# Optimization experiments

Hardware: AMD Instinct MI355X
Metric: run time of the kernel (lower is better)

The kernel has to match this reference:

```python
import jax, jax.numpy as jnp
import numpy as np

N = 50000      # nodes
E = 800000     # edges
R = 8          # relations
DIN, DH, DOUT = 128, 128, 64
EPS = 1e-5     # BatchNorm eps


def setup_inputs() -> dict:
    key = jax.random.key(0)
    ks = jax.random.split(key, 24)
    w = lambda k, shape, fan_in: jax.random.normal(k, shape, jnp.float32) / np.sqrt(fan_in)
    x = jax.random.normal(ks[0], (N, DIN), jnp.float32)
    edge_index = jax.random.randint(ks[1], (2, E), 0, N, dtype=jnp.int64)
    edge_type = jax.random.randint(ks[2], (E,), 0, R, dtype=jnp.int64)
    return {
        "x": x, "edge_index": edge_index, "edge_type": edge_type,
        # layer 1: RGCN(DIN->DH) + BN
        "W1": w(ks[3], (R, DIN, DH), DIN), "Wr1": w(ks[4], (DIN, DH), DIN), "b1": jnp.zeros((DH,), jnp.float32),
        "g1": jnp.ones((DH,), jnp.float32), "be1": jnp.zeros((DH,), jnp.float32),
        "rm1": 0.1 * jax.random.normal(ks[5], (DH,), jnp.float32),
        "rv1": jax.random.uniform(ks[6], (DH,), jnp.float32, 0.5, 1.5),
        # layer 2: RGCN(DH->DH) + BN
        "W2": w(ks[7], (R, DH, DH), DH), "Wr2": w(ks[8], (DH, DH), DH), "b2": jnp.zeros((DH,), jnp.float32),
        "g2": jnp.ones((DH,), jnp.float32), "be2": jnp.zeros((DH,), jnp.float32),
        "rm2": 0.1 * jax.random.normal(ks[9], (DH,), jnp.float32),
        "rv2": jax.random.uniform(ks[10], (DH,), jnp.float32, 0.5, 1.5),
        # layer 3: RGCN(DH->DOUT)
        "W3": w(ks[11], (R, DH, DOUT), DH), "Wr3": w(ks[12], (DH, DOUT), DH), "b3": jnp.zeros((DOUT,), jnp.float32),
    }


def rgcn_layer(x, W, Wroot, b, src, dst, et):
    # PyG RGCNConv: per-relation linear transform, per-relation MEAN aggregation
    # over incoming edges, plus root transform and bias.
    nR, nN, H = W.shape[0], x.shape[0], W.shape[2]
    h = jnp.einsum('nd,rdh->rnh', x, W)          # [R,N,H] per-relation transform
    msg = h[et, src]                             # [E,H] gather per edge
    seg = dst * nR + et                          # segment key = (node, relation)
    sums = jax.ops.segment_sum(msg, seg, num_segments=nN * nR)
    cnt = jax.ops.segment_sum(jnp.ones((seg.shape[0],), x.dtype), seg, num_segments=nN * nR)
    mean = sums / jnp.maximum(cnt, 1.0)[:, None]
    agg = mean.reshape(nN, nR, H).sum(axis=1)    # sum over relations
    return agg + x @ Wroot + b


def batchnorm(x, g, b, rm, rv):
    # eval-mode BatchNorm1d with running stats
    return (x - rm) * jax.lax.rsqrt(rv + EPS) * g + b


def reference(x, edge_index, edge_type,
              W1, Wr1, b1, g1, be1, rm1, rv1,
              W2, Wr2, b2, g2, be2, rm2, rv2,
              W3, Wr3, b3):
    src, dst = edge_index[0], edge_index[1]
    h = rgcn_layer(x, W1, Wr1, b1, src, dst, edge_type)
    h = jax.nn.relu(batchnorm(h, g1, be1, rm1, rv1))  # dropout: eval mode = identity
    h = rgcn_layer(h, W2, Wr2, b2, src, dst, edge_type)
    h = jax.nn.relu(batchnorm(h, g2, be2, rm2, rv2))
    h = rgcn_layer(h, W3, Wr3, b3, src, dst, edge_type)
    return jax.nn.sigmoid(h)
```

## Files before the change

### kernel.cpp

```cpp
#include <hip/hip_runtime.h>

typedef _Float16 f16;
typedef __attribute__((ext_vector_type(8))) _Float16 half8;
typedef __attribute__((ext_vector_type(2))) _Float16 half2v;
typedef __attribute__((ext_vector_type(4))) float float4v;

#define NNODES 50000
#define NEDGES 800000
#define NREL 8
#define NRSEG (NNODES * NREL)
#define KDIM 1152
#define CAP 16
#define CAPQ (CAP / 4)
#define NT64 ((NNODES + 63) / 64)
#define IMAX 0x7fffffff

__global__ void bucket_fill(const int* __restrict__ src, const int* __restrict__ dst,
                            const int* __restrict__ et, int* __restrict__ cnt,
                            int* __restrict__ esrc) {
    int e = blockIdx.x * blockDim.x + threadIdx.x;
    if (e < NEDGES) {
        int s = dst[e] * NREL + et[e];
        int p = atomicAdd(&cnt[s], 1);
        if (p < CAP) esrc[s * CAP + p] = src[e];
    }
}

__device__ __forceinline__ void ce(int& a, int& b) {
    int lo = min(a, b), hi = max(a, b);
    a = lo; b = hi;
}
__global__ void bucket_sort(const int* __restrict__ cnt, int* __restrict__ esrc) {
    int s = blockIdx.x * blockDim.x + threadIdx.x;
    if (s >= NRSEG) return;
    int len = cnt[s];
    len = len < CAP ? len : CAP;
    if (len < 2) return;
    int* b = esrc + (size_t)s * CAP;
    if (len <= 4) {
        int4 q = *(int4*)b;
        int v0 = q.x, v1 = len > 1 ? q.y : IMAX;
        int v2 = len > 2 ? q.z : IMAX, v3 = len > 3 ? q.w : IMAX;
        ce(v0, v1); ce(v2, v3); ce(v0, v2); ce(v1, v3); ce(v1, v2);
        *(int4*)b = (int4){v0, v1, v2, v3};
    } else if (len <= 8) {
        int4 qa = ((int4*)b)[0], qb = ((int4*)b)[1];
        int v0 = qa.x, v1 = qa.y, v2 = qa.z, v3 = qa.w;
        int v4 = qb.x, v5 = len > 5 ? qb.y : IMAX;
        int v6 = len > 6 ? qb.z : IMAX, v7 = len > 7 ? qb.w : IMAX;
        ce(v0, v1); ce(v2, v3); ce(v4, v5); ce(v6, v7);
        ce(v0, v2); ce(v1, v3); ce(v4, v6); ce(v5, v7);
        ce(v1, v2); ce(v5, v6);
        ce(v0, v4); ce(v1, v5); ce(v2, v6); ce(v3, v7);
        ce(v2, v4); ce(v3, v5);
        ce(v1, v2); ce(v3, v4); ce(v5, v6);
        ((int4*)b)[0] = (int4){v0, v1, v2, v3};
        ((int4*)b)[1] = (int4){v4, v5, v6, v7};
    } else {
        int v[CAP];
        for (int i = 0; i < len; ++i) v[i] = b[i];
        for (int i = 1; i < len; ++i) {
            int key = v[i], j = i - 1;
            while (j >= 0 && v[j] > key) { v[j + 1] = v[j]; --j; }
            v[j + 1] = key;
        }
        for (int i = 0; i < len; ++i) b[i] = v[i];
    }
}

__global__ void setup_misc(const float* __restrict__ x, f16* __restrict__ x16,
                           const float* __restrict__ W1, const float* __restrict__ Wr1,
                           const float* __restrict__ W2, const float* __restrict__ Wr2,
                           const float* __restrict__ W3, const float* __restrict__ Wr3,
                           f16* __restrict__ Bt, int* __restrict__ cnt) {
    int t = blockIdx.x * blockDim.x + threadIdx.x;
    if (t < NNODES * 64) {
        float2 v = ((const float2*)x)[t];
        half2v o = {(f16)v.x, (f16)v.y};
        ((half2v*)x16)[t] = o;
        return;
    }
    int idx = t - NNODES * 64;
    if (idx < 320 * KDIM) {
        int hg = idx / KDIM, k = idx - hg * KDIM;
        const float *W, *Wr;
        int h, H;
        if (hg < 128)      { W = W1; Wr = Wr1; h = hg;       H = 128; }
        else if (hg < 256) { W = W2; Wr = Wr2; h = hg - 128; H = 128; }
        else               { W = W3; Wr = Wr3; h = hg - 256; H = 64;  }
        float v = (k < 1024) ? W[(size_t)k * H + h] : Wr[(size_t)(k - 1024) * H + h];
        Bt[idx] = (f16)v;
        return;
    }
    int z = idx - 320 * KDIM;
    if (z < NRSEG / 4) ((int4*)cnt)[z] = (int4){0, 0, 0, 0};
}

template <int H, int HB, int MODE>
__global__ __launch_bounds__(256, 4) void fused_layer(
    const f16* __restrict__ act, const f16* __restrict__ Bt,
    const int* __restrict__ cnt, const int* __restrict__ esrc,
    const float* __restrict__ bias, const float* __restrict__ g,
    const float* __restrict__ be, const float* __restrict__ rm,
    const float* __restrict__ rv, f16* __restrict__ hout, float* __restrict__ fout) {
    constexpr int NT = HB / 16;
    __shared__ f16 Ws[HB][128];
    const int tid = threadIdx.x;
    const int wave = tid >> 6, lane = tid & 63;
    const int l15 = lane & 15, quad = lane >> 4;
    const int m0 = blockIdx.x * 64 + wave * 16;
    const int nh = blockIdx.y;
    int node = m0 + l15;
    node = node < NNODES ? node : NNODES - 1;

    int4 cq0 = ((const int4*)cnt)[node * 2];
    int4 cq1 = ((const int4*)cnt)[node * 2 + 1];
    int cnts[8] = {cq0.x, cq0.y, cq0.z, cq0.w, cq1.x, cq1.y, cq1.z, cq1.w};
    const int4* bq_base = (const int4*)esrc + (size_t)node * NREL * CAPQ;

    float4v acc[NT];
#pragma unroll
    for (int j = 0; j < NT; ++j) acc[j] = (float4v){0.f, 0.f, 0.f, 0.f};

    int4 qp0 = bq_base[0];
    int4 qp1 = bq_base[CAPQ];

#pragma unroll
    for (int r = 0; r < 9; ++r) {
        __syncthreads();
#pragma unroll
        for (int i = 0; i < NT; ++i) {
            int G = i * 256 + tid;
            int row = G >> 4, gg = G & 15;
            half8 v = *(const half8*)(Bt + (size_t)(nh * HB + row) * KDIM +
                                      r * 128 + gg * 8);
            *(half8*)&Ws[row][((gg ^ (row & 7))) * 8] = v;
        }
        half8 ch[4];
#pragma unroll
        for (int t = 0; t < 4; ++t) ch[t] = (half8)(f16)0.f;
        if (r < 8) {
            int truelen = cnts[r];
            int len = truelen < CAP ? truelen : CAP;
            f16 invh = (f16)(truelen > 1 ? 1.f / (float)truelen : 1.f);
            const int4* bq = bq_base + r * CAPQ;
            int4 q0 = qp0;
            qp0 = qp1;
            if (r < 6) qp1 = bq_base[(r + 2) * CAPQ];
            for (int j4 = 0; j4 < (len + 3) >> 2; ++j4) {
                int4 q = (j4 == 0) ? q0 : bq[j4];
                int ids[4] = {q.x, q.y, q.z, q.w};
                int base = j4 * 4;
#pragma unroll
                for (int t = 0; t < 4; ++t) {
                    if (base + t < len) {
                        const half8* rp = (const half8*)(act + (size_t)ids[t] * 128 + quad * 8);
                        half8 v0 = rp[0], v1 = rp[4], v2 = rp[8], v3 = rp[12];
                        ch[0] += v0;
                        ch[1] += v1;
                        ch[2] += v2;
                        ch[3] += v3;
                    }
                }
            }
            half8 sv;
#pragma unroll
            for (int u = 0; u < 8; ++u) sv[u] = invh;
#pragma unroll
            for (int t = 0; t < 4; ++t) ch[t] *= sv;
        } else {
#pragma unroll
            for (int ks = 0; ks < 4; ++ks)
                ch[ks] = *(const half8*)(act + (size_t)node * 128 + ks * 32 + quad * 8);
        }
        __syncthreads();
#pragma unroll
        for (int ks = 0; ks < 4; ++ks) {
#pragma unroll
            for (int nt = 0; nt < NT; ++nt) {
                int row = nt * 16 + l15;
                half8 bf = *(const half8*)&Ws[row][(((ks * 4 + quad) ^ (row & 7))) * 8];
                acc[nt] = __builtin_amdgcn_mfma_f32_16x16x32_f16(ch[ks], bf, acc[nt], 0, 0, 0);
            }
        }
    }

#pragma unroll
    for (int nt = 0; nt < NT; ++nt) {
        int col = nh * HB + nt * 16 + l15;
        float alpha, beta;
        if (MODE == 0) {
            float sc = g[col] * rsqrtf(rv[col] + 1e-5f);
            alpha = sc;
            beta = (bias[col] - rm[col]) * sc + be[col];
        } else {
            alpha = 1.f;
            beta = bias[col];
        }
#pragma unroll
        for (int rg = 0; rg < 4; ++rg) {
            int row = m0 + quad * 4 + rg;
            if (row < NNODES) {
                float v = fmaf(acc[nt][rg], alpha, beta);
                if (MODE == 0) {
                    hout[(size_t)row * H + col] = (f16)fmaxf(v, 0.f);
                } else {
                    fout[(size_t)row * H + col] = 1.f / (1.f + __expf(-v));
                }
            }
        }
    }
}

extern "C" void kernel_launch(void* const* d_in, const int* in_sizes, int n_in,
                              void* d_out, int out_size, void* d_ws, size_t ws_size,
                              hipStream_t stream) {
    (void)in_sizes; (void)n_in; (void)out_size; (void)ws_size;
    const float* x   = (const float*)d_in[0];
    const int* ei    = (const int*)d_in[1];
    const int* et    = (const int*)d_in[2];
    const float* W1  = (const float*)d_in[3];
    const float* Wr1 = (const float*)d_in[4];
    const float* b1  = (const float*)d_in[5];
    const float* g1  = (const float*)d_in[6];
    const float* be1 = (const float*)d_in[7];
    const float* rm1 = (const float*)d_in[8];
    const float* rv1 = (const float*)d_in[9];
    const float* W2  = (const float*)d_in[10];
    const float* Wr2 = (const float*)d_in[11];
    const float* b2  = (const float*)d_in[12];
    const float* g2  = (const float*)d_in[13];
    const float* be2 = (const float*)d_in[14];
    const float* rm2 = (const float*)d_in[15];
    const float* rv2 = (const float*)d_in[16];
    const float* W3  = (const float*)d_in[17];
    const float* Wr3 = (const float*)d_in[18];
    const float* b3  = (const float*)d_in[19];
    const int* src = ei;
    const int* dst = ei + NEDGES;
    float* out = (float*)d_out;

    char* ws = (char*)d_ws;
    size_t off = 0;
    auto alloc = [&](size_t bytes) -> void* {
        off = (off + 255) & ~(size_t)255;
        void* p = ws + off;
        off += bytes;
        return p;
    };
    int* cnt  = (int*)alloc((size_t)NRSEG * 4);
    int* esrc = (int*)alloc((size_t)NRSEG * CAP * 4);
    f16* x16  = (f16*)alloc((size_t)NNODES * 128 * 2);
    f16* ha   = (f16*)alloc((size_t)NNODES * 128 * 2);
    f16* hb   = (f16*)alloc((size_t)NNODES * 128 * 2);
    f16* Bt   = (f16*)alloc((size_t)320 * KDIM * 2);

    const int SETUP_T = NNODES * 64 + 320 * KDIM + NRSEG / 4;
    setup_misc<<<(SETUP_T + 255) / 256, 256, 0, stream>>>(
        x, x16, W1, Wr1, W2, Wr2, W3, Wr3, Bt, cnt);
    bucket_fill<<<(NEDGES + 255) / 256, 256, 0, stream>>>(src, dst, et, cnt, esrc);
    bucket_sort<<<(NRSEG + 255) / 256, 256, 0, stream>>>(cnt, esrc);

    fused_layer<128, 128, 0><<<dim3(NT64, 1), 256, 0, stream>>>(x16, Bt, cnt, esrc,
                                                                b1, g1, be1, rm1, rv1, ha, nullptr);
    fused_layer<128, 128, 0><<<dim3(NT64, 1), 256, 0, stream>>>(ha, Bt + (size_t)128 * KDIM, cnt, esrc,
                                                                b2, g2, be2, rm2, rv2, hb, nullptr);
    fused_layer<64, 64, 1><<<dim3(NT64, 1), 256, 0, stream>>>(hb, Bt + (size_t)256 * KDIM, cnt, esrc,
                                                              b3, nullptr, nullptr, nullptr, nullptr,
                                                              nullptr, out);
}
```

Before: 374.5 us.

## Process two relations per stage with branchless gathers from a zero pad row

```diff
diff --git a/kernel.cpp b/kernel.cpp
--- a/kernel.cpp
+++ b/kernel.cpp
@@ -72,7 +72,8 @@
                            const float* __restrict__ W1, const float* __restrict__ Wr1,
                            const float* __restrict__ W2, const float* __restrict__ Wr2,
                            const float* __restrict__ W3, const float* __restrict__ Wr3,
-                           f16* __restrict__ Bt, int* __restrict__ cnt) {
+                           f16* __restrict__ Bt, int* __restrict__ cnt,
+                           f16* __restrict__ ha, f16* __restrict__ hb) {
     int t = blockIdx.x * blockDim.x + threadIdx.x;
     if (t < NNODES * 64) {
         float2 v = ((const float2*)x)[t];
@@ -93,23 +94,32 @@
         return;
     }
     int z = idx - 320 * KDIM;
-    if (z < NRSEG / 4) ((int4*)cnt)[z] = (int4){0, 0, 0, 0};
+    if (z < NRSEG / 4) {
+        ((int4*)cnt)[z] = (int4){0, 0, 0, 0};
+        return;
+    }
+    int z2 = z - NRSEG / 4;
+    if (z2 < 48) {
+        int row = z2 >> 4, qq = z2 & 15;
+        f16* b = row == 0 ? x16 : (row == 1 ? ha : hb);
+        ((int4*)(b + (size_t)NNODES * 128))[qq] = (int4){0, 0, 0, 0};
+    }
 }
 
 template <int H, int HB, int MODE>
-__global__ __launch_bounds__(256, 4) void fused_layer(
+__global__ __launch_bounds__(256, 3) void fused_layer(
     const f16* __restrict__ act, const f16* __restrict__ Bt,
     const int* __restrict__ cnt, const int* __restrict__ esrc,
     const float* __restrict__ bias, const float* __restrict__ g,
     const float* __restrict__ be, const float* __restrict__ rm,
     const float* __restrict__ rv, f16* __restrict__ hout, float* __restrict__ fout) {
     constexpr int NT = HB / 16;
-    __shared__ f16 Ws[HB][128];
+    constexpr int GPS = HB * 16;
+    __shared__ f16 Ws[2][HB][128];
     const int tid = threadIdx.x;
     const int wave = tid >> 6, lane = tid & 63;
     const int l15 = lane & 15, quad = lane >> 4;
     const int m0 = blockIdx.x * 64 + wave * 16;
-    const int nh = blockIdx.y;
     int node = m0 + l15;
     node = node < NNODES ? node : NNODES - 1;
 
@@ -122,56 +132,78 @@
 #pragma unroll
     for (int j = 0; j < NT; ++j) acc[j] = (float4v){0.f, 0.f, 0.f, 0.f};
 
-    int4 qp0 = bq_base[0];
-    int4 qp1 = bq_base[CAPQ];
-
-#pragma unroll
-    for (int r = 0; r < 9; ++r) {
+    int4 qpA = bq_base[0];
+    int4 qpB = bq_base[CAPQ];
+
+#pragma unroll
+    for (int p = 0; p < 5; ++p) {
         __syncthreads();
-#pragma unroll
-        for (int i = 0; i < NT; ++i) {
-            int G = i * 256 + tid;
-            int row = G >> 4, gg = G & 15;
-            half8 v = *(const half8*)(Bt + (size_t)(nh * HB + row) * KDIM +
-                                      r * 128 + gg * 8);
-            *(half8*)&Ws[row][((gg ^ (row & 7))) * 8] = v;
-        }
-        half8 ch[4];
-#pragma unroll
-        for (int t = 0; t < 4; ++t) ch[t] = (half8)(f16)0.f;
-        if (r < 8) {
-            int truelen = cnts[r];
-            int len = truelen < CAP ? truelen : CAP;
-            f16 invh = (f16)(truelen > 1 ? 1.f / (float)truelen : 1.f);
-            const int4* bq = bq_base + r * CAPQ;
-            int4 q0 = qp0;
-            qp0 = qp1;
-            if (r < 6) qp1 = bq_base[(r + 2) * CAPQ];
-            for (int j4 = 0; j4 < (len + 3) >> 2; ++j4) {
-                int4 q = (j4 == 0) ? q0 : bq[j4];
-                int ids[4] = {q.x, q.y, q.z, q.w};
+        if (p < 4) {
+#pragma unroll
+            for (int i = 0; i < 2 * NT; ++i) {
+                int G = i * 256 + tid;
+                int s = G / GPS;
+                int rg = G - s * GPS;
+                int row = rg >> 4, gg = rg & 15;
+                half8 v = *(const half8*)(Bt + (size_t)row * KDIM +
+                                          (2 * p + s) * 128 + gg * 8);
+                *(half8*)&Ws[s][row][((gg ^ (row & 7))) * 8] = v;
+            }
+        } else {
+#pragma unroll
+            for (int i = 0; i < NT; ++i) {
+                int G = i * 256 + tid;
+                int row = G >> 4, gg = G & 15;
+                half8 v = *(const half8*)(Bt + (size_t)row * KDIM + 1024 + gg * 8);
+                *(half8*)&Ws[0][row][((gg ^ (row & 7))) * 8] = v;
+            }
+        }
+        half8 chA[4], chB[4];
+#pragma unroll
+        for (int t = 0; t < 4; ++t) { chA[t] = (half8)(f16)0.f; chB[t] = (half8)(f16)0.f; }
+        if (p < 4) {
+            int ra = 2 * p, rb = 2 * p + 1;
+            int tlA = cnts[ra], tlB = cnts[rb];
+            int lenA = tlA < CAP ? tlA : CAP;
+            int lenB = tlB < CAP ? tlB : CAP;
+            f16 invA = (f16)(tlA > 1 ? 1.f / (float)tlA : 1.f);
+            f16 invB = (f16)(tlB > 1 ? 1.f / (float)tlB : 1.f);
+            const int4* bqA = bq_base + ra * CAPQ;
+            const int4* bqB = bq_base + rb * CAPQ;
+            int4 qa0 = qpA, qb0 = qpB;
+            if (p < 3) {
+                qpA = bq_base[(2 * p + 2) * CAPQ];
+                qpB = bq_base[(2 * p + 3) * CAPQ];
+            }
+            int lenM = lenA > lenB ? lenA : lenB;
+            for (int j4 = 0; j4 < (lenM + 3) >> 2; ++j4) {
+                int4 qa = (j4 == 0) ? qa0 : bqA[j4];
+                int4 qb = (j4 == 0) ? qb0 : bqB[j4];
+                int ia[4] = {qa.x, qa.y, qa.z, qa.w};
+                int ib[4] = {qb.x, qb.y, qb.z, qb.w};
                 int base = j4 * 4;
 #pragma unroll
                 for (int t = 0; t < 4; ++t) {
-                    if (base + t < len) {
-                        const half8* rp = (const half8*)(act + (size_t)ids[t] * 128 + quad * 8);
-                        half8 v0 = rp[0], v1 = rp[4], v2 = rp[8], v3 = rp[12];
-                        ch[0] += v0;
-                        ch[1] += v1;
-                        ch[2] += v2;
-                        ch[3] += v3;
-                    }
+                    int e = base + t;
+                    int iA = e < lenA ? ia[t] : NNODES;
+                    int iB = e < lenB ? ib[t] : NNODES;
+                    const half8* pA = (const half8*)(act + (size_t)iA * 128 + quad * 8);
+                    const half8* pB = (const half8*)(act + (size_t)iB * 128 + quad * 8);
+                    half8 a0 = pA[0], a1 = pA[4], a2 = pA[8], a3 = pA[12];
+                    half8 b0 = pB[0], b1 = pB[4], b2 = pB[8], b3 = pB[12];
+                    chA[0] += a0; chA[1] += a1; chA[2] += a2; chA[3] += a3;
+                    chB[0] += b0; chB[1] += b1; chB[2] += b2; chB[3] += b3;
                 }
             }
-            half8 sv;
-#pragma unroll
-            for (int u = 0; u < 8; ++u) sv[u] = invh;
-#pragma unroll
-            for (int t = 0; t < 4; ++t) ch[t] *= sv;
+            half8 svA, svB;
+#pragma unroll
+            for (int u = 0; u < 8; ++u) { svA[u] = invA; svB[u] = invB; }
+#pragma unroll
+            for (int t = 0; t < 4; ++t) { chA[t] *= svA; chB[t] *= svB; }
         } else {
 #pragma unroll
             for (int ks = 0; ks < 4; ++ks)
-                ch[ks] = *(const half8*)(act + (size_t)node * 128 + ks * 32 + quad * 8);
+                chA[ks] = *(const half8*)(act + (size_t)node * 128 + ks * 32 + quad * 8);
         }
         __syncthreads();
 #pragma unroll
@@ -179,15 +211,26 @@
 #pragma unroll
             for (int nt = 0; nt < NT; ++nt) {
                 int row = nt * 16 + l15;
-                half8 bf = *(const half8*)&Ws[row][(((ks * 4 + quad) ^ (row & 7))) * 8];
-                acc[nt] = __builtin_amdgcn_mfma_f32_16x16x32_f16(ch[ks], bf, acc[nt], 0, 0, 0);
+                half8 bf = *(const half8*)&Ws[0][row][(((ks * 4 + quad) ^ (row & 7))) * 8];
+                acc[nt] = __builtin_amdgcn_mfma_f32_16x16x32_f16(chA[ks], bf, acc[nt], 0, 0, 0);
+            }
+        }
+        if (p < 4) {
+#pragma unroll
+            for (int ks = 0; ks < 4; ++ks) {
+#pragma unroll
+                for (int nt = 0; nt < NT; ++nt) {
+                    int row = nt * 16 + l15;
+                    half8 bf = *(const half8*)&Ws[1][row][(((ks * 4 + quad) ^ (row & 7))) * 8];
+                    acc[nt] = __builtin_amdgcn_mfma_f32_16x16x32_f16(chB[ks], bf, acc[nt], 0, 0, 0);
+                }
             }
         }
     }
 
 #pragma unroll
     for (int nt = 0; nt < NT; ++nt) {
-        int col = nh * HB + nt * 16 + l15;
+        int col = nt * 16 + l15;
         float alpha, beta;
         if (MODE == 0) {
             float sc = g[col] * rsqrtf(rv[col] + 1e-5f);
@@ -250,14 +293,14 @@
     };
     int* cnt  = (int*)alloc((size_t)NRSEG * 4);
     int* esrc = (int*)alloc((size_t)NRSEG * CAP * 4);
-    f16* x16  = (f16*)alloc((size_t)NNODES * 128 * 2);
-    f16* ha   = (f16*)alloc((size_t)NNODES * 128 * 2);
-    f16* hb   = (f16*)alloc((size_t)NNODES * 128 * 2);
+    f16* x16  = (f16*)alloc((size_t)(NNODES + 1) * 128 * 2);
+    f16* ha   = (f16*)alloc((size_t)(NNODES + 1) * 128 * 2);
+    f16* hb   = (f16*)alloc((size_t)(NNODES + 1) * 128 * 2);
     f16* Bt   = (f16*)alloc((size_t)320 * KDIM * 2);
 
-    const int SETUP_T = NNODES * 64 + 320 * KDIM + NRSEG / 4;
+    const int SETUP_T = NNODES * 64 + 320 * KDIM + NRSEG / 4 + 48;
     setup_misc<<<(SETUP_T + 255) / 256, 256, 0, stream>>>(
-        x, x16, W1, Wr1, W2, Wr2, W3, Wr3, Bt, cnt);
+        x, x16, W1, Wr1, W2, Wr2, W3, Wr3, Bt, cnt, ha, hb);
     bucket_fill<<<(NEDGES + 255) / 256, 256, 0, stream>>>(src, dst, et, cnt, esrc);
     bucket_sort<<<(NRSEG + 255) / 256, 256, 0, stream>>>(cnt, esrc);
 
```

New measurement: 487.5 us. 30.2% more time.

## Split output columns across blocks and preload all weight slices into LDS

Applied to the files above, without the earlier changes.

```diff
diff --git a/kernel.cpp b/kernel.cpp
--- a/kernel.cpp
+++ b/kernel.cpp
@@ -72,7 +72,8 @@
                            const float* __restrict__ W1, const float* __restrict__ Wr1,
                            const float* __restrict__ W2, const float* __restrict__ Wr2,
                            const float* __restrict__ W3, const float* __restrict__ Wr3,
-                           f16* __restrict__ Bt, int* __restrict__ cnt) {
+                           f16* __restrict__ Bt, int* __restrict__ cnt,
+                           f16* __restrict__ ha, f16* __restrict__ hb) {
     int t = blockIdx.x * blockDim.x + threadIdx.x;
     if (t < NNODES * 64) {
         float2 v = ((const float2*)x)[t];
@@ -93,18 +94,29 @@
         return;
     }
     int z = idx - 320 * KDIM;
-    if (z < NRSEG / 4) ((int4*)cnt)[z] = (int4){0, 0, 0, 0};
+    if (z < NRSEG / 4) {
+        ((int4*)cnt)[z] = (int4){0, 0, 0, 0};
+        return;
+    }
+    int z2 = z - NRSEG / 4;
+    if (z2 < 48) {
+        int row = z2 >> 4, qq = z2 & 15;
+        f16* b = row == 0 ? x16 : (row == 1 ? ha : hb);
+        ((int4*)(b + (size_t)NNODES * 128))[qq] = (int4){0, 0, 0, 0};
+    }
 }
 
 template <int H, int HB, int MODE>
-__global__ __launch_bounds__(256, 4) void fused_layer(
+__global__ __launch_bounds__(256, 2) void fused_layer(
     const f16* __restrict__ act, const f16* __restrict__ Bt,
     const int* __restrict__ cnt, const int* __restrict__ esrc,
     const float* __restrict__ bias, const float* __restrict__ g,
     const float* __restrict__ be, const float* __restrict__ rm,
     const float* __restrict__ rv, f16* __restrict__ hout, float* __restrict__ fout) {
     constexpr int NT = HB / 16;
-    __shared__ f16 Ws[HB][128];
+    constexpr int GPS = HB * 16;
+    constexpr int ITER = 9 * GPS / 256;
+    __shared__ f16 Ws[9][HB][128];
     const int tid = threadIdx.x;
     const int wave = tid >> 6, lane = tid & 63;
     const int l15 = lane & 15, quad = lane >> 4;
@@ -113,6 +125,17 @@
     int node = m0 + l15;
     node = node < NNODES ? node : NNODES - 1;
 
+#pragma unroll
+    for (int i = 0; i < ITER; ++i) {
+        int G = i * 256 + tid;
+        int s = G / GPS;
+        int rem = G - s * GPS;
+        int row = rem >> 4, gg = rem & 15;
+        half8 v = *(const half8*)(Bt + (size_t)(nh * HB + row) * KDIM +
+                                  s * 128 + gg * 8);
+        *(half8*)&Ws[s][row][((gg ^ (row & 7))) * 8] = v;
+    }
+
     int4 cq0 = ((const int4*)cnt)[node * 2];
     int4 cq1 = ((const int4*)cnt)[node * 2 + 1];
     int cnts[8] = {cq0.x, cq0.y, cq0.z, cq0.w, cq1.x, cq1.y, cq1.z, cq1.w};
@@ -122,20 +145,10 @@
 #pragma unroll
     for (int j = 0; j < NT; ++j) acc[j] = (float4v){0.f, 0.f, 0.f, 0.f};
 
-    int4 qp0 = bq_base[0];
-    int4 qp1 = bq_base[CAPQ];
+    __syncthreads();
 
 #pragma unroll
     for (int r = 0; r < 9; ++r) {
-        __syncthreads();
-#pragma unroll
-        for (int i = 0; i < NT; ++i) {
-            int G = i * 256 + tid;
-            int row = G >> 4, gg = G & 15;
-            half8 v = *(const half8*)(Bt + (size_t)(nh * HB + row) * KDIM +
-                                      r * 128 + gg * 8);
-            *(half8*)&Ws[row][((gg ^ (row & 7))) * 8] = v;
-        }
         half8 ch[4];
 #pragma unroll
         for (int t = 0; t < 4; ++t) ch[t] = (half8)(f16)0.f;
@@ -144,11 +157,8 @@
             int len = truelen < CAP ? truelen : CAP;
             f16 invh = (f16)(truelen > 1 ? 1.f / (float)truelen : 1.f);
             const int4* bq = bq_base + r * CAPQ;
-            int4 q0 = qp0;
-            qp0 = qp1;
-            if (r < 6) qp1 = bq_base[(r + 2) * CAPQ];
             for (int j4 = 0; j4 < (len + 3) >> 2; ++j4) {
-                int4 q = (j4 == 0) ? q0 : bq[j4];
+                int4 q = bq[j4];
                 int ids[4] = {q.x, q.y, q.z, q.w};
                 int base = j4 * 4;
 #pragma unroll
@@ -173,13 +183,12 @@
             for (int ks = 0; ks < 4; ++ks)
                 ch[ks] = *(const half8*)(act + (size_t)node * 128 + ks * 32 + quad * 8);
         }
-        __syncthreads();
 #pragma unroll
         for (int ks = 0; ks < 4; ++ks) {
 #pragma unroll
             for (int nt = 0; nt < NT; ++nt) {
                 int row = nt * 16 + l15;
-                half8 bf = *(const half8*)&Ws[row][(((ks * 4 + quad) ^ (row & 7))) * 8];
+                half8 bf = *(const half8*)&Ws[r][row][(((ks * 4 + quad) ^ (row & 7))) * 8];
                 acc[nt] = __builtin_amdgcn_mfma_f32_16x16x32_f16(ch[ks], bf, acc[nt], 0, 0, 0);
             }
         }
@@ -250,22 +259,22 @@
     };
     int* cnt  = (int*)alloc((size_t)NRSEG * 4);
     int* esrc = (int*)alloc((size_t)NRSEG * CAP * 4);
-    f16* x16  = (f16*)alloc((size_t)NNODES * 128 * 2);
-    f16* ha   = (f16*)alloc((size_t)NNODES * 128 * 2);
-    f16* hb   = (f16*)alloc((size_t)NNODES * 128 * 2);
+    f16* x16  = (f16*)alloc((size_t)(NNODES + 1) * 128 * 2);
+    f16* ha   = (f16*)alloc((size_t)(NNODES + 1) * 128 * 2);
+    f16* hb   = (f16*)alloc((size_t)(NNODES + 1) * 128 * 2);
     f16* Bt   = (f16*)alloc((size_t)320 * KDIM * 2);
 
-    const int SETUP_T = NNODES * 64 + 320 * KDIM + NRSEG / 4;
+    const int SETUP_T = NNODES * 64 + 320 * KDIM + NRSEG / 4 + 48;
     setup_misc<<<(SETUP_T + 255) / 256, 256, 0, stream>>>(
-        x, x16, W1, Wr1, W2, Wr2, W3, Wr3, Bt, cnt);
+        x, x16, W1, Wr1, W2, Wr2, W3, Wr3, Bt, cnt, ha, hb);
     bucket_fill<<<(NEDGES + 255) / 256, 256, 0, stream>>>(src, dst, et, cnt, esrc);
     bucket_sort<<<(NRSEG + 255) / 256, 256, 0, stream>>>(cnt, esrc);
 
-    fused_layer<128, 128, 0><<<dim3(NT64, 1), 256, 0, stream>>>(x16, Bt, cnt, esrc,
-                                                                b1, g1, be1, rm1, rv1, ha, nullptr);
-    fused_layer<128, 128, 0><<<dim3(NT64, 1), 256, 0, stream>>>(ha, Bt + (size_t)128 * KDIM, cnt, esrc,
-                                                                b2, g2, be2, rm2, rv2, hb, nullptr);
-    fused_layer<64, 64, 1><<<dim3(NT64, 1), 256, 0, stream>>>(hb, Bt + (size_t)256 * KDIM, cnt, esrc,
+    fused_layer<128, 32, 0><<<dim3(NT64, 4), 256, 0, stream>>>(x16, Bt, cnt, esrc,
+                                                               b1, g1, be1, rm1, rv1, ha, nullptr);
+    fused_layer<128, 32, 0><<<dim3(NT64, 4), 256, 0, stream>>>(ha, Bt + (size_t)128 * KDIM, cnt, esrc,
+                                                               b2, g2, be2, rm2, rv2, hb, nullptr);
+    fused_layer<64, 32, 1><<<dim3(NT64, 2), 256, 0, stream>>>(hb, Bt + (size_t)256 * KDIM, cnt, esrc,
                                                               b3, nullptr, nullptr, nullptr, nullptr,
                                                               nullptr, out);
 }
```

After: 690.5 us. 1.84x slower.
